# Kernel tuning notes

Measured on AMD Instinct MI355X. Metric: run time of the kernel, lower is better.

Reference implementation:

```python
import jax, jax.numpy as jnp
import numpy as np

H, KVH, HD, E, TOPK = 16, 4, 128, 8, 2
EPS = 1.1920929e-07  # fp32 machine eps, matches F.rms_norm default


def _rms(v):
    return v * jax.lax.rsqrt(jnp.mean(jnp.square(v), axis=-1, keepdims=True) + EPS)


def _rope(t, cos, sin):
    d = t.shape[-1] // 2
    t1, t2 = t[..., :d], t[..., d:]
    return jnp.concatenate([t1 * cos + t2 * sin, -t1 * sin + t2 * cos], axis=-1)


def setup_inputs():
    key = jax.random.key(0)
    ks = jax.random.split(key, 10)
    B, T, C, D = 2, 1024, 2048, 512
    # real rotary tables (broadcast over batch and heads)
    inv = 1.0 / (10000.0 ** (np.arange(HD // 2, dtype=np.float64) / (HD // 2)))
    ang = np.arange(T, dtype=np.float64)[:, None] * inv[None, :]
    cos = jnp.asarray(np.cos(ang), jnp.float32)[None, :, None, :]
    sin = jnp.asarray(np.sin(ang), jnp.float32)[None, :, None, :]
    w = lambda k, shp, fan: jax.random.normal(k, shp, jnp.float32) * (fan ** -0.5)
    return {
        'x': jax.random.normal(ks[0], (B, T, C), jnp.float32),
        'cos': cos, 'sin': sin,
        'Wq': w(ks[1], (C, C), C),
        'Wk': w(ks[2], (C, KVH * HD), C),
        'Wv': w(ks[3], (C, KVH * HD), C),
        'Wo': w(ks[4], (C, C), C),
        'Wr': w(ks[5], (C, E), C),
        'Ws1': w(ks[6], (C, D), C),
        'Ws2': w(ks[7], (D, C), D),
        'We1': w(ks[8], (E, C, D), C),
        'We2': w(ks[9], (E, D, C), D),
    }


def reference(x, cos, sin, Wq, Wk, Wv, Wo, Wr, Ws1, Ws2, We1, We2):
    B, T, C = x.shape
    # ---- attention (pre-norm, RoPE, QK-norm, GQA, causal SDPA) ----
    xn = _rms(x)
    q = _rms(_rope((xn @ Wq).reshape(B, T, H, HD), cos, sin))      # [B,T,H,HD]
    k = _rms(_rope((xn @ Wk).reshape(B, T, KVH, HD), cos, sin))    # [B,T,KVH,HD]
    v = (xn @ Wv).reshape(B, T, KVH, HD)
    rep = H // KVH
    k = jnp.repeat(k, rep, axis=2)
    v = jnp.repeat(v, rep, axis=2)
    scores = jnp.einsum('bthd,bshd->bhts', q, k) / np.float32(np.sqrt(HD))
    causal = jnp.tril(jnp.ones((T, T), bool))
    scores = jnp.where(causal, scores, jnp.float32(-np.inf))
    att = jax.nn.softmax(scores, axis=-1)
    y = jnp.einsum('bhts,bshd->bthd', att, v).reshape(B, T, C) @ Wo
    x = x + y
    # ---- DeepSeekMoE (shared expert + top-k routed experts) ----
    xf = _rms(x).reshape(-1, C)                                    # [N,C]
    N = xf.shape[0]
    shared = jnp.square(jax.nn.relu(xf @ Ws1)) @ Ws2               # [N,C]
    logits = xf @ Wr                                               # [N,E]
    tk_w, tk_idx = jax.lax.top_k(logits, TOPK)
    tk_w = jax.nn.softmax(tk_w.astype(jnp.float32), axis=-1).astype(x.dtype)
    # scatter top-k probs into dense per-expert gates (indices unique per row)
    gates = jnp.zeros((N, E), x.dtype).at[jnp.arange(N)[:, None], tk_idx].set(tk_w)
    h = jnp.square(jax.nn.relu(jnp.einsum('nc,ecd->end', xf, We1)))  # [E,N,D]
    routed = jnp.einsum('end,edc,ne->nc', h, We2, gates)             # [N,C]
    return x + (shared + routed).reshape(B, T, C)
```

## Files before the change

kernel.cpp:

```cpp
#include <hip/hip_runtime.h>

typedef _Float16 h16;
typedef _Float16 half8 __attribute__((ext_vector_type(8)));
typedef float f32x4 __attribute__((ext_vector_type(4)));

#define EPS_RMS 1.1920929e-07f
#define MiB (1ull << 20)

__device__ __forceinline__ void gload_lds16(const void* g, void* l) {
  __builtin_amdgcn_global_load_lds(
      (const __attribute__((address_space(1))) unsigned int*)g,
      (__attribute__((address_space(3))) unsigned int*)l, 16, 0, 0);
}

struct GemmP {
  const h16* Ah; const h16* Al;
  const h16* Bh; const h16* Bl;
  float* Cf; h16* Ch; h16* Cl;
  const float* R;
  const int* cnt; const int* off; const int* perm;
  long sAz, sBz, sCzHi, sCzLo;
  int M, N, K, lda, ldb, ldc;
  int zAoff, zBoff, zCoff, bzShift, czHiShift, czLoMask;
  float outScale;
};

template <int SPLIT, int EPI, int USECNT, int GATHER, int ASYNC>
__global__ __launch_bounds__(256, 4) void gemm_k(GemmP p) {
  constexpr int NP = SPLIT ? 2 : 1;
  constexpr int APAD = (ASYNC == 1) ? 32 : 40;
  constexpr int BPAD = (ASYNC >= 1) ? 32 : 40;
  __shared__ __align__(16) h16 As[NP][128][APAD];
  __shared__ __align__(16) h16 Bs[NP][128][BPAD];
  __shared__ int permLds[GATHER ? 128 : 1];

  const int nwg = gridDim.x * gridDim.y;
  const int flat = blockIdx.y * gridDim.x + blockIdx.x;
  const int q8 = nwg >> 3, r8 = nwg & 7;
  const int xcd = flat & 7, sub = flat >> 3;
  const int swz = (xcd < r8 ? xcd * (q8 + 1) : r8 * (q8 + 1) + (xcd - r8) * q8) + sub;
  const int bm = swz % gridDim.x, bn = swz / gridDim.x;
  const int zl = blockIdx.z;

  int Meff, rowbase;
  if (USECNT) {
    Meff = p.cnt[zl]; rowbase = p.off[zl];
    if (bm * 128 >= Meff) return;
  } else { Meff = p.M; rowbase = 0; }

  const int zA = zl + p.zAoff, zB = zl + p.zBoff, zC = zl + p.zCoff;
  const h16* Ah = p.Ah + (size_t)zA * p.sAz;
  const h16* Al = SPLIT ? p.Al + (size_t)zA * p.sAz : (const h16*)0;
  const size_t bofs = (size_t)(zB >> p.bzShift) * p.sBz;
  const h16* Bh = p.Bh + bofs;
  const h16* Bl = SPLIT ? p.Bl + bofs : (const h16*)0;
  const size_t cofs = (size_t)(zC >> p.czHiShift) * p.sCzHi +
                      (size_t)(zC & p.czLoMask) * p.sCzLo;

  const int tid = threadIdx.x;
  const int lane = tid & 63;
  const int wid = tid >> 6, wr = wid >> 1, wc = wid & 1;
  const int fr = lane & 15, fq = lane >> 4;

  if (GATHER) {
    if (tid < 128) {
      const int local = bm * 128 + tid;
      permLds[tid] = (local < Meff) ? p.perm[rowbase + local] : -1;
    }
    __syncthreads();
  }

  const long arow0 = (long)rowbase + (long)bm * 128;

  const f32x4 fz = {0.f, 0.f, 0.f, 0.f};
  f32x4 acc[4][4];
#pragma unroll
  for (int m = 0; m < 4; ++m)
#pragma unroll
    for (int n = 0; n < 4; ++n) acc[m][n] = fz;

  const int nkt = p.K / 32;

  for (int kt = 0; kt < nkt; ++kt) {
    if (kt) __syncthreads();
    const int kb = kt * 32;
    if constexpr (ASYNC >= 1) {
#pragma unroll
      for (int it = 0; it < 2; ++it) {
        const int d = (tid + it * 256) * 16;
        const int row = d >> 6;
        const int oct = (d >> 4) & 3;
        const size_t gb = ((size_t)(bn * 128 + row)) * p.ldb + kb + oct * 8;
        gload_lds16(Bh + gb, (char*)&Bs[0][0][0] + d);
        if (SPLIT) gload_lds16(Bl + gb, (char*)&Bs[1][0][0] + d);
        if constexpr (ASYNC == 1) {
          const size_t ga = (size_t)(arow0 + row) * p.lda + kb + oct * 8;
          gload_lds16(Ah + ga, (char*)&As[0][0][0] + d);
          if (SPLIT) gload_lds16(Al + ga, (char*)&As[1][0][0] + d);
        }
      }
    }
    if constexpr (ASYNC != 1) {
#pragma unroll
      for (int s = 0; s < 2; ++s) {
        const int seg = tid * 2 + s;
        const int row = seg >> 2, ks = (seg & 3) * 8;
        const int local = bm * 128 + row;
        bool av; long arow;
        if (GATHER) { const int tk2 = permLds[row]; av = (tk2 >= 0); arow = tk2; }
        else { av = (local < Meff); arow = (long)rowbase + local; }
        half8 vh = {0,0,0,0,0,0,0,0}, vl = {0,0,0,0,0,0,0,0};
        if (av) {
          vh = *(const half8*)(Ah + arow * (size_t)p.lda + kb + ks);
          if (SPLIT) vl = *(const half8*)(Al + arow * (size_t)p.lda + kb + ks);
        }
        *(half8*)&As[0][row][ks] = vh;
        if (SPLIT) *(half8*)&As[1][row][ks] = vl;
        if constexpr (ASYNC == 0) {
          const long brow = (long)bn * 128 + row;
          *(half8*)&Bs[0][row][ks] = *(const half8*)(Bh + brow * (size_t)p.ldb + kb + ks);
          if (SPLIT)
            *(half8*)&Bs[1][row][ks] = *(const half8*)(Bl + brow * (size_t)p.ldb + kb + ks);
        }
      }
    }
    __syncthreads();

    half8 af[NP][4], bf[NP][4];
#pragma unroll
    for (int m = 0; m < 4; ++m) {
      const int r = wr * 64 + m * 16 + fr;
      af[0][m] = *(const half8*)&As[0][r][fq * 8];
      if (SPLIT) af[1][m] = *(const half8*)&As[1][r][fq * 8];
    }
#pragma unroll
    for (int n = 0; n < 4; ++n) {
      const int c = wc * 64 + n * 16 + fr;
      bf[0][n] = *(const half8*)&Bs[0][c][fq * 8];
      if (SPLIT) bf[1][n] = *(const half8*)&Bs[1][c][fq * 8];
    }
#pragma unroll
    for (int m = 0; m < 4; ++m)
#pragma unroll
      for (int n = 0; n < 4; ++n) {
        acc[m][n] = __builtin_amdgcn_mfma_f32_16x16x32_f16(af[0][m], bf[0][n], acc[m][n], 0, 0, 0);
        if (SPLIT) {
          acc[m][n] = __builtin_amdgcn_mfma_f32_16x16x32_f16(af[0][m], bf[1][n], acc[m][n], 0, 0, 0);
          acc[m][n] = __builtin_amdgcn_mfma_f32_16x16x32_f16(af[1][m], bf[0][n], acc[m][n], 0, 0, 0);
        }
      }
  }

#pragma unroll
  for (int m = 0; m < 4; ++m)
#pragma unroll
    for (int n = 0; n < 4; ++n)
#pragma unroll
      for (int j = 0; j < 4; ++j) {
        const int rl = wr * 64 + m * 16 + fq * 4 + j;
        const int cl = wc * 64 + n * 16 + fr;
        const int local = bm * 128 + rl;
        if (local >= Meff) continue;
        const size_t idx = cofs + ((size_t)rowbase + local) * p.ldc + (size_t)bn * 128 + cl;
        const float v = acc[m][n][j] * p.outScale;
        if (EPI == 0) p.Cf[idx] = v;
        else if (EPI == 1) p.Cf[idx] = v + p.R[idx];
        else if (EPI == 2) {
          const h16 hh = (h16)v;
          p.Ch[idx] = hh; p.Cl[idx] = (h16)(v - (float)hh);
        } else if (EPI == 3) {
          const float r2 = v > 0.f ? v * v : 0.f;
          p.Ch[idx] = (h16)r2;
        } else {
          p.Ch[idx] = (h16)v;
        }
      }
}

__global__ __launch_bounds__(512, 1) void flash_k(
    const h16* __restrict__ Qh, const h16* __restrict__ Ql,
    const h16* __restrict__ Kh, const h16* __restrict__ Kl,
    const h16* __restrict__ Vh, const h16* __restrict__ Vl,
    h16* __restrict__ yh, h16* __restrict__ yl) {
  __shared__ __align__(16) h16 Ks[2][32][136];
  __shared__ __align__(16) h16 Vs[2][128][40];
  __shared__ __align__(16) h16 Ps[8][2][16][40];

  const int qb = blockIdx.x, z = blockIdx.y;
  const int b = z >> 4, h = z & 15;
  const size_t qoff = (size_t)z * 131072;
  const size_t koff = (size_t)(b * 4 + (h >> 2)) * 131072;

  const int tid = threadIdx.x;
  const int lane = tid & 63, w = tid >> 6;
  const int fr = lane & 15, fq = lane >> 4;

  const int qrow = qb * 128 + w * 16 + fr;
  half8 qa[2][4];
#pragma unroll
  for (int kt = 0; kt < 4; ++kt) {
    qa[0][kt] = *(const half8*)(Qh + qoff + (size_t)qrow * 128 + kt * 32 + fq * 8);
    qa[1][kt] = *(const half8*)(Ql + qoff + (size_t)qrow * 128 + kt * 32 + fq * 8);
  }

  const int kRow = tid >> 4, kSeg = tid & 15;
  const int vRow = tid >> 2, vSeg = tid & 3;

  const f32x4 fz = {0.f, 0.f, 0.f, 0.f};
  f32x4 y[8];
#pragma unroll
  for (int n = 0; n < 8; ++n) y[n] = fz;
  float mrow[4] = {-3.0e38f, -3.0e38f, -3.0e38f, -3.0e38f};
  float lrow[4] = {0.f, 0.f, 0.f, 0.f};

  const int nt = (qb + 1) * 4;
  for (int t = 0; t < nt; ++t) {
    const int kvb = t * 32;
    if (t) __syncthreads();
#pragma unroll
    for (int pl = 0; pl < 2; ++pl) {
      const h16* kp = pl ? Kl : Kh;
      const h16* vp = pl ? Vl : Vh;
      *(half8*)&Ks[pl][kRow][kSeg * 8] =
          *(const half8*)(kp + koff + (size_t)(kvb + kRow) * 128 + kSeg * 8);
      *(half8*)&Vs[pl][vRow][vSeg * 8] =
          *(const half8*)(vp + koff + (size_t)vRow * 1024 + kvb + vSeg * 8);
    }
    __syncthreads();

    f32x4 sf[2] = {fz, fz};
#pragma unroll
    for (int n = 0; n < 2; ++n)
#pragma unroll
      for (int kt = 0; kt < 4; ++kt) {
        const half8 bh2 = *(const half8*)&Ks[0][n * 16 + fr][kt * 32 + fq * 8];
        const half8 bl2 = *(const half8*)&Ks[1][n * 16 + fr][kt * 32 + fq * 8];
        sf[n] = __builtin_amdgcn_mfma_f32_16x16x32_f16(qa[0][kt], bh2, sf[n], 0, 0, 0);
        sf[n] = __builtin_amdgcn_mfma_f32_16x16x32_f16(qa[0][kt], bl2, sf[n], 0, 0, 0);
        sf[n] = __builtin_amdgcn_mfma_f32_16x16x32_f16(qa[1][kt], bh2, sf[n], 0, 0, 0);
      }

    if (kvb + 31 > qb * 128) {
#pragma unroll
      for (int n = 0; n < 2; ++n)
#pragma unroll
        for (int j = 0; j < 4; ++j) {
          const int kvg = kvb + n * 16 + fr;
          const int qg = qb * 128 + w * 16 + fq * 4 + j;
          if (kvg > qg) sf[n][j] = -3.0e38f;
        }
    }

    float al[4];
#pragma unroll
    for (int j = 0; j < 4; ++j) {
      float tm = fmaxf(sf[0][j], sf[1][j]);
#pragma unroll
      for (int msk = 1; msk < 16; msk <<= 1) tm = fmaxf(tm, __shfl_xor(tm, msk, 16));
      const float mn = fmaxf(mrow[j], tm);
      al[j] = __expf(mrow[j] - mn);
      mrow[j] = mn;
      sf[0][j] = __expf(sf[0][j] - mn);
      sf[1][j] = __expf(sf[1][j] - mn);
      float ts = sf[0][j] + sf[1][j];
#pragma unroll
      for (int msk = 1; msk < 16; msk <<= 1) ts += __shfl_xor(ts, msk, 16);
      lrow[j] = lrow[j] * al[j] + ts;
    }
#pragma unroll
    for (int n = 0; n < 8; ++n)
#pragma unroll
      for (int j = 0; j < 4; ++j) y[n][j] *= al[j];

#pragma unroll
    for (int n = 0; n < 2; ++n)
#pragma unroll
      for (int j = 0; j < 4; ++j) {
        const float pp = sf[n][j] * 1024.f;
        const h16 hh = (h16)pp;
        Ps[w][0][fq * 4 + j][n * 16 + fr] = hh;
        Ps[w][1][fq * 4 + j][n * 16 + fr] = (h16)(pp - (float)hh);
      }

    const half8 pah = *(const half8*)&Ps[w][0][fr][fq * 8];
    const half8 pal = *(const half8*)&Ps[w][1][fr][fq * 8];
#pragma unroll
    for (int n = 0; n < 8; ++n) {
      const half8 vh2 = *(const half8*)&Vs[0][n * 16 + fr][fq * 8];
      const half8 vl2 = *(const half8*)&Vs[1][n * 16 + fr][fq * 8];
      y[n] = __builtin_amdgcn_mfma_f32_16x16x32_f16(pah, vh2, y[n], 0, 0, 0);
      y[n] = __builtin_amdgcn_mfma_f32_16x16x32_f16(pah, vl2, y[n], 0, 0, 0);
      y[n] = __builtin_amdgcn_mfma_f32_16x16x32_f16(pal, vh2, y[n], 0, 0, 0);
    }
  }

#pragma unroll
  for (int n = 0; n < 8; ++n)
#pragma unroll
    for (int j = 0; j < 4; ++j) {
      const int row = qb * 128 + w * 16 + fq * 4 + j;
      const int col = h * 128 + n * 16 + fr;
      const float v = y[n][j] / (1024.f * lrow[j]);
      const size_t idx = ((size_t)(b * 1024 + row)) * 2048 + col;
      const h16 hh = (h16)v;
      yh[idx] = hh; yl[idx] = (h16)(v - (float)hh);
    }
}

__global__ void tsplit_k(const float* __restrict__ W, h16* __restrict__ Th,
                         h16* __restrict__ Tl, int K, int N, float scale, int wantLo) {
  const size_t eoff = (size_t)blockIdx.z * (size_t)K * N;
  W += eoff; Th += eoff; if (Tl) Tl += eoff;
  __shared__ float tile[32][33];
  const int nt = blockIdx.x * 32, kt = blockIdx.y * 32;
  const int c = threadIdx.x & 31, r0 = threadIdx.x >> 5;
#pragma unroll
  for (int rr = 0; rr < 4; ++rr)
    tile[r0 + rr * 8][c] = W[(size_t)(kt + r0 + rr * 8) * N + nt + c];
  __syncthreads();
#pragma unroll
  for (int rr = 0; rr < 4; ++rr) {
    const int nrow = nt + r0 + rr * 8;
    const float v = tile[c][r0 + rr * 8] * scale;
    const h16 hh = (h16)v;
    Th[(size_t)nrow * K + kt + c] = hh;
    if (wantLo) Tl[(size_t)nrow * K + kt + c] = (h16)(v - (float)hh);
  }
}

template <int WLO, int WSC>
__global__ void rms_k(const float* __restrict__ X, h16* __restrict__ H,
                      h16* __restrict__ L, float* __restrict__ SC) {
  const int row = blockIdx.x;
  const float* x = X + (size_t)row * 2048;
  __shared__ float red[256];
  const int tid = threadIdx.x;
  float ss = 0.f;
  for (int c = tid; c < 2048; c += 256) { const float v = x[c]; ss += v * v; }
  red[tid] = ss; __syncthreads();
  for (int t = 128; t > 0; t >>= 1) {
    if (tid < t) red[tid] += red[tid + t];
    __syncthreads();
  }
  const float sc = rsqrtf(red[0] * (1.f / 2048.f) + EPS_RMS);
  if (WSC && tid == 0) SC[row] = sc;
  for (int c = tid; c < 2048; c += 256) {
    const float v = x[c] * sc;
    const size_t o2 = (size_t)row * 2048 + c;
    const h16 hh = (h16)v;
    H[o2] = hh;
    if (WLO) L[o2] = (h16)(v - (float)hh);
  }
}

__global__ void rope_k(const float* __restrict__ qkv, const float* __restrict__ cosT,
                       const float* __restrict__ sinT,
                       h16* __restrict__ Qh, h16* __restrict__ Ql,
                       h16* __restrict__ Kh, h16* __restrict__ Kl,
                       h16* __restrict__ Vh, h16* __restrict__ Vl) {
  const int tok = blockIdx.x;
  const int b = tok >> 10, t = tok & 1023;
  const int u = blockIdx.y, d = threadIdx.x;
  __shared__ float buf[128];
  __shared__ float red[128];
  int col;
  if (u < 16) col = u * 128 + d;
  else if (u < 20) col = 2048 + (u - 16) * 128 + d;
  else col = 2560 + (u - 20) * 128 + d;
  float v = qkv[(size_t)tok * 3072 + col];
  if (u < 20) {
    buf[d] = v; __syncthreads();
    float r;
    if (d < 64) {
      const float c = cosT[t * 64 + d], s = sinT[t * 64 + d];
      r = buf[d] * c + buf[d + 64] * s;
    } else {
      const float c = cosT[t * 64 + d - 64], s = sinT[t * 64 + d - 64];
      r = -buf[d - 64] * s + buf[d] * c;
    }
    red[d] = r * r; __syncthreads();
    for (int tt = 64; tt > 0; tt >>= 1) {
      if (d < tt) red[d] += red[d + tt];
      __syncthreads();
    }
    v = r * rsqrtf(red[0] * (1.f / 128.f) + EPS_RMS);
    if (u < 16) v *= 0.08838834764831845f;
  }
  const h16 hh = (h16)v;
  const h16 lo = (h16)(v - (float)hh);
  if (u < 16) {
    const size_t o2 = (((size_t)(b * 16 + u)) * 1024 + t) * 128 + d;
    Qh[o2] = hh; Ql[o2] = lo;
  } else if (u < 20) {
    const size_t o2 = (((size_t)(b * 4 + (u - 16))) * 1024 + t) * 128 + d;
    Kh[o2] = hh; Kl[o2] = lo;
  } else {
    const size_t o2 = ((size_t)(b * 4 + (u - 20))) * 131072 + (size_t)d * 1024 + t;
    Vh[o2] = hh; Vl[o2] = lo;
  }
}

__global__ void router_k(const float* __restrict__ x2, const float* __restrict__ rowscale,
                         const float* __restrict__ Wr,
                         int* __restrict__ idx2, float* __restrict__ g2,
                         int* __restrict__ cnt) {
  const int n = blockIdx.x;
  const int tid = threadIdx.x;
  __shared__ float red[256][8];
  float part[8] = {0, 0, 0, 0, 0, 0, 0, 0};
  for (int c = tid; c < 2048; c += 256) {
    const float v = x2[(size_t)n * 2048 + c];
    const float* w2 = Wr + (size_t)c * 8;
#pragma unroll
    for (int e = 0; e < 8; ++e) part[e] += v * w2[e];
  }
#pragma unroll
  for (int e = 0; e < 8; ++e) red[tid][e] = part[e];
  __syncthreads();
  for (int t = 128; t > 0; t >>= 1) {
    if (tid < t)
#pragma unroll
      for (int e = 0; e < 8; ++e) red[tid][e] += red[tid + t][e];
    __syncthreads();
  }
  if (tid == 0) {
    const float sc = rowscale[n];
    float l[8];
#pragma unroll
    for (int e = 0; e < 8; ++e) l[e] = red[0][e] * sc;
    int i1 = 0;
    for (int e = 1; e < 8; ++e) if (l[e] > l[i1]) i1 = e;
    int i2 = (i1 == 0) ? 1 : 0;
    for (int e = 0; e < 8; ++e) if (e != i1 && l[e] > l[i2]) i2 = e;
    const float e2 = __expf(l[i2] - l[i1]);
    const float inv = 1.f / (1.f + e2);
    idx2[n * 2] = i1; idx2[n * 2 + 1] = i2;
    g2[n * 2] = inv; g2[n * 2 + 1] = e2 * inv;
    atomicAdd(&cnt[i1], 1); atomicAdd(&cnt[i2], 1);
  }
}

__global__ void zero8_k(int* __restrict__ p) {
  if (threadIdx.x < 8 && blockIdx.x == 0) p[threadIdx.x] = 0;
}

__global__ void scan_k(const int* __restrict__ cnt, int* __restrict__ off,
                       int* __restrict__ base) {
  if (threadIdx.x == 0 && blockIdx.x == 0) {
    int a = 0;
    for (int e = 0; e < 8; ++e) { off[e] = a; base[e] = a; a += cnt[e]; }
  }
}

__global__ void assign_k(const int* __restrict__ idx2, int* __restrict__ base,
                         int* __restrict__ perm, int* __restrict__ pos2) {
  const int n = blockIdx.x * 256 + threadIdx.x;
  if (n >= 2048) return;
  for (int j = 0; j < 2; ++j) {
    const int e = idx2[n * 2 + j];
    const int pos = atomicAdd(&base[e], 1);
    perm[pos] = n;
    pos2[n * 2 + j] = pos;
  }
}

__global__ void combine_k(const float* __restrict__ x2, const h16* __restrict__ sh,
                          const h16* __restrict__ rp, const int* __restrict__ pos2,
                          const float* __restrict__ g2, float* __restrict__ out) {
  const int n = blockIdx.x;
  const int p0 = pos2[n * 2], p1 = pos2[n * 2 + 1];
  const float g0 = g2[n * 2], g1 = g2[n * 2 + 1];
  for (int c = threadIdx.x; c < 2048; c += 256) {
    const size_t i = (size_t)n * 2048 + c;
    out[i] = x2[i] + (float)sh[i] + g0 * (float)rp[(size_t)p0 * 2048 + c]
             + g1 * (float)rp[(size_t)p1 * 2048 + c];
  }
}

extern "C" void kernel_launch(void* const* d_in, const int* in_sizes, int n_in,
                              void* d_out, int out_size, void* d_ws, size_t ws_size,
                              hipStream_t stream) {
  const float* x    = (const float*)d_in[0];
  const float* cosT = (const float*)d_in[1];
  const float* sinT = (const float*)d_in[2];
  const float* Wq   = (const float*)d_in[3];
  const float* Wk   = (const float*)d_in[4];
  const float* Wv   = (const float*)d_in[5];
  const float* Wo   = (const float*)d_in[6];
  const float* Wr   = (const float*)d_in[7];
  const float* Ws1  = (const float*)d_in[8];
  const float* Ws2  = (const float*)d_in[9];
  const float* We1  = (const float*)d_in[10];
  const float* We2  = (const float*)d_in[11];
  float* out = (float*)d_out;

  unsigned char* W = (unsigned char*)d_ws;
  int*   idx2     = (int*)(W + 0);
  float* g2       = (float*)(W + 16 * 1024);
  int*   cnt      = (int*)(W + 32 * 1024);
  int*   offs     = (int*)(W + 33 * 1024);
  int*   base     = (int*)(W + 34 * 1024);
  int*   perm     = (int*)(W + 36 * 1024);
  int*   pos2     = (int*)(W + 52 * 1024);
  float* rowscale = (float*)(W + 68 * 1024);
  h16* W1h = (h16*)(W + 1 * MiB);
  h16* W1l = (h16*)(W + 13 * MiB);
  h16* W2h = (h16*)(W + 1 * MiB);
  h16* W2l = (h16*)(W + 9 * MiB);
  h16* xnh = (h16*)(W + 25 * MiB);
  h16* xnl = (h16*)(W + 33 * MiB);
  h16* yh  = (h16*)(W + 25 * MiB);
  h16* yl  = (h16*)(W + 33 * MiB);
  h16* xfh = (h16*)(W + 25 * MiB);
  h16* shh = (h16*)(W + 33 * MiB);
  float* qkv = (float*)(W + 41 * MiB);
  h16* hs    = (h16*)(W + 41 * MiB);
  h16* hperm = (h16*)(W + 43 * MiB);
  h16* Qh = (h16*)(W + 65 * MiB);
  h16* Ql = (h16*)(W + 73 * MiB);
  h16* Kh = (h16*)(W + 81 * MiB);
  h16* Kl = (h16*)(W + 83 * MiB);
  h16* Vh = (h16*)(W + 85 * MiB);
  h16* Vl = (h16*)(W + 87 * MiB);
  h16* rph = (h16*)(W + 65 * MiB);
  float* x2 = (float*)(W + 89 * MiB);
  h16* Ws1T = (h16*)(W + 105 * MiB);
  h16* Ws2T = (h16*)(W + 107 * MiB);
  h16* WeT  = (h16*)(W + 109 * MiB);

  const float WS = 64.f;
  const float IWS = 1.f / 64.f;

  tsplit_k<<<dim3(64, 64, 1), 256, 0, stream>>>(Wq, W1h, W1l, 2048, 2048, WS, 1);
  tsplit_k<<<dim3(16, 64, 1), 256, 0, stream>>>(Wk, W1h + (size_t)2048 * 2048,
                                                W1l + (size_t)2048 * 2048, 2048, 512, WS, 1);
  tsplit_k<<<dim3(16, 64, 1), 256, 0, stream>>>(Wv, W1h + (size_t)2560 * 2048,
                                                W1l + (size_t)2560 * 2048, 2048, 512, WS, 1);
  zero8_k<<<1, 64, 0, stream>>>(cnt);
  rms_k<1, 0><<<2048, 256, 0, stream>>>(x, xnh, xnl, (float*)0);
  {
    GemmP p{};
    p.Ah = xnh; p.Al = xnl; p.Bh = W1h; p.Bl = W1l; p.Cf = qkv;
    p.M = 2048; p.N = 3072; p.K = 2048; p.lda = 2048; p.ldb = 2048; p.ldc = 3072;
    p.outScale = IWS;
    gemm_k<1, 0, 0, 0, 1><<<dim3(16, 24, 1), 256, 0, stream>>>(p);
  }

  rope_k<<<dim3(2048, 24, 1), 128, 0, stream>>>(qkv, cosT, sinT, Qh, Ql, Kh, Kl, Vh, Vl);

  tsplit_k<<<dim3(64, 64, 1), 256, 0, stream>>>(Wo, W2h, W2l, 2048, 2048, WS, 1);
  flash_k<<<dim3(8, 32, 1), 512, 0, stream>>>(Qh, Ql, Kh, Kl, Vh, Vl, yh, yl);

  {
    GemmP p{};
    p.Ah = yh; p.Al = yl; p.Bh = W2h; p.Bl = W2l; p.Cf = x2; p.R = x;
    p.M = 2048; p.N = 2048; p.K = 2048; p.lda = 2048; p.ldb = 2048; p.ldc = 2048;
    p.outScale = IWS;
    gemm_k<1, 1, 0, 0, 1><<<dim3(16, 16, 1), 256, 0, stream>>>(p);
  }

  rms_k<0, 1><<<2048, 256, 0, stream>>>(x2, xfh, (h16*)0, rowscale);
  router_k<<<2048, 256, 0, stream>>>(x2, rowscale, Wr, idx2, g2, cnt);
  scan_k<<<1, 64, 0, stream>>>(cnt, offs, base);
  assign_k<<<8, 256, 0, stream>>>(idx2, base, perm, pos2);

  tsplit_k<<<dim3(16, 64, 1), 256, 0, stream>>>(Ws1, Ws1T, (h16*)0, 2048, 512, WS, 0);
  tsplit_k<<<dim3(64, 16, 1), 256, 0, stream>>>(Ws2, Ws2T, (h16*)0, 512, 2048, WS, 0);
  {
    GemmP p{};
    p.Ah = xfh; p.Bh = Ws1T; p.Ch = hs;
    p.M = 2048; p.N = 512; p.K = 2048; p.lda = 2048; p.ldb = 2048; p.ldc = 512;
    p.outScale = IWS;
    gemm_k<0, 3, 0, 0, 1><<<dim3(16, 4, 1), 256, 0, stream>>>(p);
  }
  {
    GemmP p{};
    p.Ah = hs; p.Bh = Ws2T; p.Ch = shh;
    p.M = 2048; p.N = 2048; p.K = 512; p.lda = 512; p.ldb = 512; p.ldc = 2048;
    p.outScale = IWS;
    gemm_k<0, 4, 0, 0, 1><<<dim3(16, 16, 1), 256, 0, stream>>>(p);
  }
  tsplit_k<<<dim3(16, 64, 8), 256, 0, stream>>>(We1, WeT, (h16*)0, 2048, 512, WS, 0);
  {
    GemmP p{};
    p.Ah = xfh; p.Bh = WeT; p.Ch = hperm;
    p.M = 2048; p.N = 512; p.K = 2048; p.lda = 2048; p.ldb = 2048; p.ldc = 512;
    p.sBz = (long)512 * 2048; p.bzShift = 0;
    p.cnt = cnt; p.off = offs; p.perm = perm;
    p.outScale = IWS;
    gemm_k<0, 3, 1, 1, 2><<<dim3(16, 4, 8), 256, 0, stream>>>(p);
  }
  tsplit_k<<<dim3(64, 16, 8), 256, 0, stream>>>(We2, WeT, (h16*)0, 512, 2048, WS, 0);
  {
    GemmP p{};
    p.Ah = hperm; p.Bh = WeT; p.Cf = (float*)0; p.Ch = rph;
    p.M = 2048; p.N = 2048; p.K = 512; p.lda = 512; p.ldb = 512; p.ldc = 2048;
    p.sBz = (long)2048 * 512; p.bzShift = 0;
    p.cnt = cnt; p.off = offs; p.perm = perm;
    p.outScale = IWS;
    gemm_k<0, 4, 1, 0, 1><<<dim3(16, 16, 8), 256, 0, stream>>>(p);
  }

  combine_k<<<2048, 256, 0, stream>>>(x2, shh, rph, pos2, g2, out);
}
```

Before: 590.4 us.

## Double-buffer async LDS loads in GEMM and remap grouped-expert block indexing

For the fully asynchronous path (ASYNC==1), the GEMM now keeps two LDS buffers and issues the global-to-LDS loads for the next K tile before computing the current one. This is meant to hide load latency behind the MFMA work. It doubles the shared memory used by that variant, which may lower occupancy under launch_bounds(256,4). For the grouped (USECNT) expert GEMMs it also replaces the XCD swizzle with a mapping that spreads experts across the low bits of the flat block id, so each expert's tiles are distributed over the XCDs.

```diff
diff --git a/kernel.cpp b/kernel.cpp
--- a/kernel.cpp
+++ b/kernel.cpp
@@ -28,19 +28,30 @@
 template <int SPLIT, int EPI, int USECNT, int GATHER, int ASYNC>
 __global__ __launch_bounds__(256, 4) void gemm_k(GemmP p) {
   constexpr int NP = SPLIT ? 2 : 1;
+  constexpr int NBUF = (ASYNC == 1) ? 2 : 1;
   constexpr int APAD = (ASYNC == 1) ? 32 : 40;
   constexpr int BPAD = (ASYNC >= 1) ? 32 : 40;
-  __shared__ __align__(16) h16 As[NP][128][APAD];
-  __shared__ __align__(16) h16 Bs[NP][128][BPAD];
+  __shared__ __align__(16) h16 As[NBUF][NP][128][APAD];
+  __shared__ __align__(16) h16 Bs[NBUF][NP][128][BPAD];
   __shared__ int permLds[GATHER ? 128 : 1];
 
-  const int nwg = gridDim.x * gridDim.y;
-  const int flat = blockIdx.y * gridDim.x + blockIdx.x;
-  const int q8 = nwg >> 3, r8 = nwg & 7;
-  const int xcd = flat & 7, sub = flat >> 3;
-  const int swz = (xcd < r8 ? xcd * (q8 + 1) : r8 * (q8 + 1) + (xcd - r8) * q8) + sub;
-  const int bm = swz % gridDim.x, bn = swz / gridDim.x;
-  const int zl = blockIdx.z;
+  int bm, bn, zl;
+  if constexpr (USECNT) {
+    const int flat2d = blockIdx.y * gridDim.x + blockIdx.x;
+    zl = flat2d & 7;
+    const int idx = (flat2d >> 3) * 8 + blockIdx.z;
+    bm = idx % gridDim.x;
+    bn = idx / gridDim.x;
+  } else {
+    const int nwg = gridDim.x * gridDim.y;
+    const int flat = blockIdx.y * gridDim.x + blockIdx.x;
+    const int q8 = nwg >> 3, r8 = nwg & 7;
+    const int xcd = flat & 7, sub = flat >> 3;
+    const int swz = (xcd < r8 ? xcd * (q8 + 1) : r8 * (q8 + 1) + (xcd - r8) * q8) + sub;
+    bm = swz % gridDim.x;
+    bn = swz / gridDim.x;
+    zl = blockIdx.z;
+  }
 
   int Meff, rowbase;
   if (USECNT) {
@@ -81,26 +92,72 @@
 
   const int nkt = p.K / 32;
 
-  for (int kt = 0; kt < nkt; ++kt) {
-    if (kt) __syncthreads();
-    const int kb = kt * 32;
-    if constexpr (ASYNC >= 1) {
+  auto compute = [&](int buf) {
+    half8 af[NP][4], bf[NP][4];
+#pragma unroll
+    for (int m = 0; m < 4; ++m) {
+      const int r = wr * 64 + m * 16 + fr;
+      af[0][m] = *(const half8*)&As[buf][0][r][fq * 8];
+      if (SPLIT) af[1][m] = *(const half8*)&As[buf][1][r][fq * 8];
+    }
+#pragma unroll
+    for (int n = 0; n < 4; ++n) {
+      const int c = wc * 64 + n * 16 + fr;
+      bf[0][n] = *(const half8*)&Bs[buf][0][c][fq * 8];
+      if (SPLIT) bf[1][n] = *(const half8*)&Bs[buf][1][c][fq * 8];
+    }
+#pragma unroll
+    for (int m = 0; m < 4; ++m)
+#pragma unroll
+      for (int n = 0; n < 4; ++n) {
+        acc[m][n] = __builtin_amdgcn_mfma_f32_16x16x32_f16(af[0][m], bf[0][n], acc[m][n], 0, 0, 0);
+        if (SPLIT) {
+          acc[m][n] = __builtin_amdgcn_mfma_f32_16x16x32_f16(af[0][m], bf[1][n], acc[m][n], 0, 0, 0);
+          acc[m][n] = __builtin_amdgcn_mfma_f32_16x16x32_f16(af[1][m], bf[0][n], acc[m][n], 0, 0, 0);
+        }
+      }
+  };
+
+  if constexpr (ASYNC == 1) {
+    auto stage = [&](int buf, int kt) {
+      const int kb = kt * 32;
 #pragma unroll
       for (int it = 0; it < 2; ++it) {
         const int d = (tid + it * 256) * 16;
         const int row = d >> 6;
         const int oct = (d >> 4) & 3;
         const size_t gb = ((size_t)(bn * 128 + row)) * p.ldb + kb + oct * 8;
-        gload_lds16(Bh + gb, (char*)&Bs[0][0][0] + d);
-        if (SPLIT) gload_lds16(Bl + gb, (char*)&Bs[1][0][0] + d);
-        if constexpr (ASYNC == 1) {
-          const size_t ga = (size_t)(arow0 + row) * p.lda + kb + oct * 8;
-          gload_lds16(Ah + ga, (char*)&As[0][0][0] + d);
-          if (SPLIT) gload_lds16(Al + ga, (char*)&As[1][0][0] + d);
+        gload_lds16(Bh + gb, (char*)&Bs[buf][0][0][0] + d);
+        if (SPLIT) gload_lds16(Bl + gb, (char*)&Bs[buf][1][0][0] + d);
+        const size_t ga = (size_t)(arow0 + row) * p.lda + kb + oct * 8;
+        gload_lds16(Ah + ga, (char*)&As[buf][0][0][0] + d);
+        if (SPLIT) gload_lds16(Al + ga, (char*)&As[buf][1][0][0] + d);
+      }
+    };
+    stage(0, 0);
+    __syncthreads();
+    int cur = 0;
+    for (int kt = 0; kt < nkt; ++kt) {
+      if (kt + 1 < nkt) stage(cur ^ 1, kt + 1);
+      compute(cur);
+      __syncthreads();
+      cur ^= 1;
+    }
+  } else {
+    for (int kt = 0; kt < nkt; ++kt) {
+      if (kt) __syncthreads();
+      const int kb = kt * 32;
+      if constexpr (ASYNC == 2) {
+#pragma unroll
+        for (int it = 0; it < 2; ++it) {
+          const int d = (tid + it * 256) * 16;
+          const int row = d >> 6;
+          const int oct = (d >> 4) & 3;
+          const size_t gb = ((size_t)(bn * 128 + row)) * p.ldb + kb + oct * 8;
+          gload_lds16(Bh + gb, (char*)&Bs[0][0][0][0] + d);
+          if (SPLIT) gload_lds16(Bl + gb, (char*)&Bs[0][1][0][0] + d);
         }
       }
-    }
-    if constexpr (ASYNC != 1) {
 #pragma unroll
       for (int s = 0; s < 2; ++s) {
         const int seg = tid * 2 + s;
@@ -114,41 +171,18 @@
           vh = *(const half8*)(Ah + arow * (size_t)p.lda + kb + ks);
           if (SPLIT) vl = *(const half8*)(Al + arow * (size_t)p.lda + kb + ks);
         }
-        *(half8*)&As[0][row][ks] = vh;
-        if (SPLIT) *(half8*)&As[1][row][ks] = vl;
+        *(half8*)&As[0][0][row][ks] = vh;
+        if (SPLIT) *(half8*)&As[0][1][row][ks] = vl;
         if constexpr (ASYNC == 0) {
           const long brow = (long)bn * 128 + row;
-          *(half8*)&Bs[0][row][ks] = *(const half8*)(Bh + brow * (size_t)p.ldb + kb + ks);
+          *(half8*)&Bs[0][0][row][ks] = *(const half8*)(Bh + brow * (size_t)p.ldb + kb + ks);
           if (SPLIT)
-            *(half8*)&Bs[1][row][ks] = *(const half8*)(Bl + brow * (size_t)p.ldb + kb + ks);
+            *(half8*)&Bs[0][1][row][ks] = *(const half8*)(Bl + brow * (size_t)p.ldb + kb + ks);
         }
       }
-    }
-    __syncthreads();
-
-    half8 af[NP][4], bf[NP][4];
-#pragma unroll
-    for (int m = 0; m < 4; ++m) {
-      const int r = wr * 64 + m * 16 + fr;
-      af[0][m] = *(const half8*)&As[0][r][fq * 8];
-      if (SPLIT) af[1][m] = *(const half8*)&As[1][r][fq * 8];
-    }
-#pragma unroll
-    for (int n = 0; n < 4; ++n) {
-      const int c = wc * 64 + n * 16 + fr;
-      bf[0][n] = *(const half8*)&Bs[0][c][fq * 8];
-      if (SPLIT) bf[1][n] = *(const half8*)&Bs[1][c][fq * 8];
-    }
-#pragma unroll
-    for (int m = 0; m < 4; ++m)
-#pragma unroll
-      for (int n = 0; n < 4; ++n) {
-        acc[m][n] = __builtin_amdgcn_mfma_f32_16x16x32_f16(af[0][m], bf[0][n], acc[m][n], 0, 0, 0);
-        if (SPLIT) {
-          acc[m][n] = __builtin_amdgcn_mfma_f32_16x16x32_f16(af[0][m], bf[1][n], acc[m][n], 0, 0, 0);
-          acc[m][n] = __builtin_amdgcn_mfma_f32_16x16x32_f16(af[1][m], bf[0][n], acc[m][n], 0, 0, 0);
-        }
-      }
+      __syncthreads();
+      compute(0);
+    }
   }
 
 #pragma unroll
```

Measured after the change: 585.2 us. Within noise of the previous version (-0.9%).
